# Kernel optimization log

Measured on AMD Instinct MI355X. Metric: run time of the kernel, lower is better.

Reference implementation:

```python
import jax, jax.numpy as jnp
import numpy as np

N = 50000       # num nodes
E = 800000      # num edges (avg degree 16)
D_IN = 128
D_H = 128
D_LAT = 64
BN_EPS = 1e-5


def _glorot(key, fan_in, fan_out):
    return jax.random.normal(key, (fan_in, fan_out), jnp.float32) / np.sqrt(fan_in).astype(np.float32)


def setup_inputs() -> dict:
    key = jax.random.key(0)
    ks = jax.random.split(key, 8)
    x = jax.random.normal(ks[0], (N, D_IN), jnp.float32)
    edge_index = jax.random.randint(ks[1], (2, E), 0, N)  # row 0 = src, row 1 = dst
    return {
        "x": x,
        "edge_index": edge_index,
        "W0": _glorot(ks[2], D_IN, D_H),
        "W1": _glorot(ks[3], D_H, D_H),
        "W_mu": _glorot(ks[4], D_H, D_LAT),
        "W_logvar": _glorot(ks[5], D_H, D_LAT),
        "gamma0": jnp.ones((D_H,), jnp.float32),
        "beta0": jnp.zeros((D_H,), jnp.float32),
        "gamma1": jnp.ones((D_H,), jnp.float32),
        "beta1": jnp.zeros((D_H,), jnp.float32),
    }


def _gcn_conv(h, W, src, dst, dinv):
    # Standard GCN with self-loops: D^{-1/2}(A+I)D^{-1/2} (X W)
    m = h @ W                                   # [N, out]
    coef = (dinv[src] * dinv[dst])[:, None]     # [E, 1]
    out = jax.ops.segment_sum(m[src] * coef, dst, num_segments=N)
    return out + m * (dinv * dinv)[:, None]     # self-loop contribution


def _batchnorm(h, gamma, beta):
    mean = jnp.mean(h, axis=0)
    var = jnp.var(h, axis=0)
    return (h - mean) * jax.lax.rsqrt(var + BN_EPS) * gamma + beta


def reference(x, edge_index, W0, W1, W_mu, W_logvar, gamma0, beta0, gamma1, beta1):
    # decoder_type='graph', augment_type=None, used_edge_weight=False,
    # use_FCencoder=False, num_domains=1; dropout is identity in reference.
    src, dst = edge_index[0], edge_index[1]
    deg = jax.ops.segment_sum(jnp.ones((E,), x.dtype), dst, num_segments=N) + 1.0
    dinv = jax.lax.rsqrt(deg)

    h = _gcn_conv(x, W0, src, dst, dinv)
    h = jax.nn.relu(_batchnorm(h, gamma0, beta0))
    h = _gcn_conv(h, W1, src, dst, dinv)
    h = jax.nn.relu(_batchnorm(h, gamma1, beta1))

    z_mean = _gcn_conv(h, W_mu, src, dst, dinv)
    z_log_std = _gcn_conv(h, W_logvar, src, dst, dinv)
    return (z_mean, z_log_std)
```

## Files before the change

### kernel.cpp

```cpp
#include <hip/hip_runtime.h>
#include <hip/hip_bf16.h>


using short8 = __attribute__((ext_vector_type(8))) short;
using f32x4  = __attribute__((ext_vector_type(4))) float;

static __device__ __forceinline__ unsigned short f2bf(float f) {
    __hip_bfloat16 h = __float2bfloat16(f);
    return *reinterpret_cast<unsigned short*>(&h);
}
static __device__ __forceinline__ float bf_lo(unsigned int u) {
    return __uint_as_float(u << 16);
}
static __device__ __forceinline__ float bf_hi(unsigned int u) {
    return __uint_as_float(u & 0xffff0000u);
}
static __device__ __forceinline__ float bf2f(unsigned short u) {
    return __uint_as_float((unsigned int)u << 16);
}

__global__ __launch_bounds__(256)
void deg_count(const int* __restrict__ ei, int* __restrict__ cnt, int E_) {
    int e = blockIdx.x * 256 + threadIdx.x;
    if (e < E_) atomicAdd(&cnt[ei[E_ + e]], 1);
}

__global__ __launch_bounds__(1024)
void scan_blocks(const int* __restrict__ cnt, float* __restrict__ dinv,
                 int* __restrict__ rowptr, int* __restrict__ partials, int n) {
    __shared__ int ls[1024];
    int tid = threadIdx.x;
    int i = blockIdx.x * 1024 + tid;
    int v = (i < n) ? cnt[i] : 0;
    if (i < n) dinv[i] = rsqrtf((float)v + 1.0f);
    ls[tid] = v;
    __syncthreads();
    #pragma unroll
    for (int off = 1; off < 1024; off <<= 1) {
        int t = (tid >= off) ? ls[tid - off] : 0;
        __syncthreads();
        ls[tid] += t;
        __syncthreads();
    }
    if (i < n) rowptr[i] = ls[tid] - v;
    if (tid == 1023) partials[blockIdx.x] = ls[1023];
}

__global__ __launch_bounds__(1024)
void scan_partials(int* __restrict__ partials, int* __restrict__ rowptr_n,
                   int nb) {
    __shared__ int ls[1024];
    int tid = threadIdx.x;
    int v = (tid < nb) ? partials[tid] : 0;
    ls[tid] = v;
    __syncthreads();
    #pragma unroll
    for (int off = 1; off < 1024; off <<= 1) {
        int t = (tid >= off) ? ls[tid - off] : 0;
        __syncthreads();
        ls[tid] += t;
        __syncthreads();
    }
    if (tid < nb) partials[tid] = ls[tid] - v;
    if (tid == 1023) *rowptr_n = ls[1023];
}

__global__ __launch_bounds__(256)
void scan_add(int* __restrict__ rowptr, int* __restrict__ cursor,
              const int* __restrict__ partials, int n) {
    int i = blockIdx.x * 256 + threadIdx.x;
    if (i < n) {
        int v = rowptr[i] + partials[i >> 10];
        rowptr[i] = v;
        cursor[i] = v;
    }
}

__global__ __launch_bounds__(256)
void csr_fill(const int* __restrict__ ei, const float* __restrict__ dinv,
              int* __restrict__ cursor, unsigned int* __restrict__ csr, int E_) {
    int e = blockIdx.x * 256 + threadIdx.x;
    if (e >= E_) return;
    int s = ei[e], d = ei[E_ + e];
    float coef = dinv[s] * dinv[d];
    unsigned int cb = (__float_as_uint(coef) + 0x8000u) >> 16;
    int p = atomicAdd(&cursor[d], 1);
    csr[p] = ((unsigned int)s << 15) | (cb & 0x7fffu);
}

__global__ __launch_bounds__(128)
void bn_coef(const float* __restrict__ stats, const float* __restrict__ gamma,
             const float* __restrict__ beta, float* __restrict__ sc,
             float* __restrict__ sh, int n) {
    int c = threadIdx.x;
    float inv_n = 1.0f / (float)n;
    float mean = stats[c] * inv_n;
    float var  = stats[128 + c] * inv_n - mean * mean;
    float s = rsqrtf(var + 1e-5f) * gamma[c];
    sc[c] = s;
    sh[c] = beta[c] - mean * s;
}

template<bool XBF, bool FUSE_BN, bool SPLIT_W>
__global__ __launch_bounds__(256)
void gemm_mfma(const void* __restrict__ Xv, const float* __restrict__ Wa,
               const float* __restrict__ Wb, const float* __restrict__ sc,
               const float* __restrict__ sh, unsigned short* __restrict__ Y,
               int nRows) {
    __shared__ unsigned short wt[128 * 128];

    const int tid = threadIdx.x;

    #pragma unroll
    for (int it = 0; it < 16; ++it) {
        int flat4 = it * 256 + tid;
        int k  = flat4 >> 5;
        int c0 = (flat4 & 31) * 4;
        const float* srcp;
        if (!SPLIT_W) srcp = Wa + k * 128 + c0;
        else          srcp = (c0 < 64) ? (Wa + k * 64 + c0)
                                       : (Wb + k * 64 + (c0 - 64));
        float4 v = *(const float4*)srcp;
        float vv[4] = {v.x, v.y, v.z, v.w};
        #pragma unroll
        for (int j = 0; j < 4; ++j) {
            int c = c0 + j;
            wt[c * 128 + (k ^ ((c & 7) << 3))] = f2bf(vv[j]);
        }
    }
    __syncthreads();

    const int lane = tid & 63;
    const int wv   = tid >> 6;
    const int lm   = lane & 15;
    const int lg   = lane >> 4;
    const int row0 = blockIdx.x * 128 + wv * 32;

    f32x4 acc[2][8] = {};

    #pragma unroll
    for (int ks = 0; ks < 4; ++ks) {
        const int k0 = ks * 32 + lg * 8;

        short8 a[2];
        #pragma unroll
        for (int mf = 0; mf < 2; ++mf) {
            int r = row0 + mf * 16 + lm;
            if (r < nRows) {
                if (XBF) {
                    a[mf] = *(const short8*)((const unsigned short*)Xv +
                                             (size_t)r * 128 + k0);
                    if (FUSE_BN) {
                        float4 s0 = *(const float4*)(sc + k0);
                        float4 s1 = *(const float4*)(sc + k0 + 4);
                        float4 h0 = *(const float4*)(sh + k0);
                        float4 h1 = *(const float4*)(sh + k0 + 4);
                        float sv[8] = {s0.x, s0.y, s0.z, s0.w, s1.x, s1.y, s1.z, s1.w};
                        float hv[8] = {h0.x, h0.y, h0.z, h0.w, h1.x, h1.y, h1.z, h1.w};
                        #pragma unroll
                        for (int j = 0; j < 8; ++j) {
                            float v = bf2f((unsigned short)a[mf][j]);
                            v = fmaxf(v * sv[j] + hv[j], 0.f);
                            a[mf][j] = (short)f2bf(v);
                        }
                    }
                } else {
                    const float* xp = (const float*)Xv + (size_t)r * 128 + k0;
                    float4 p0 = *(const float4*)xp;
                    float4 p1 = *(const float4*)(xp + 4);
                    float pv[8] = {p0.x, p0.y, p0.z, p0.w, p1.x, p1.y, p1.z, p1.w};
                    #pragma unroll
                    for (int j = 0; j < 8; ++j) a[mf][j] = (short)f2bf(pv[j]);
                }
            } else {
                a[mf] = short8{};
            }
        }

        #pragma unroll
        for (int f = 0; f < 8; ++f) {
            int c = f * 16 + lm;
            short8 b = *(const short8*)&wt[c * 128 + (k0 ^ ((c & 7) << 3))];
            acc[0][f] = __builtin_amdgcn_mfma_f32_16x16x32_bf16(a[0], b, acc[0][f], 0, 0, 0);
            acc[1][f] = __builtin_amdgcn_mfma_f32_16x16x32_bf16(a[1], b, acc[1][f], 0, 0, 0);
        }
    }

    #pragma unroll
    for (int mf = 0; mf < 2; ++mf) {
        #pragma unroll
        for (int reg = 0; reg < 4; ++reg) {
            int r = row0 + mf * 16 + lg * 4 + reg;
            if (r >= nRows) continue;
            #pragma unroll
            for (int f = 0; f < 8; ++f)
                Y[(size_t)r * 128 + f * 16 + lm] = f2bf(acc[mf][f][reg]);
        }
    }
}

template<bool TO_OUT>
__global__ __launch_bounds__(256)
void gather_bf(const unsigned short* __restrict__ M,
               const int* __restrict__ rowptr,
               const unsigned int* __restrict__ csr,
               const float* __restrict__ dinv, void* __restrict__ O, int n) {
    int wid  = (blockIdx.x * 256 + threadIdx.x) >> 6;
    int lane = threadIdx.x & 63;
    if (wid >= n) return;
    const unsigned int* m2 = (const unsigned int*)M;

    float di = dinv[wid];
    unsigned int su = m2[(size_t)wid * 64 + lane];
    float c = di * di;
    float a0x = bf_lo(su) * c, a0y = bf_hi(su) * c;
    float a1x = 0.f, a1y = 0.f, a2x = 0.f, a2y = 0.f, a3x = 0.f, a3y = 0.f;

    int beg = __builtin_amdgcn_readfirstlane(rowptr[wid]);
    int end = __builtin_amdgcn_readfirstlane(rowptr[wid + 1]);

    int k = beg;
    for (; k + 3 < end; k += 4) {
        unsigned int e0 = csr[k],     e1 = csr[k + 1];
        unsigned int e2 = csr[k + 2], e3 = csr[k + 3];
        unsigned int u0 = m2[(size_t)(e0 >> 15) * 64 + lane];
        unsigned int u1 = m2[(size_t)(e1 >> 15) * 64 + lane];
        unsigned int u2 = m2[(size_t)(e2 >> 15) * 64 + lane];
        unsigned int u3 = m2[(size_t)(e3 >> 15) * 64 + lane];
        float w0 = __uint_as_float((e0 & 0x7fffu) << 16);
        float w1 = __uint_as_float((e1 & 0x7fffu) << 16);
        float w2 = __uint_as_float((e2 & 0x7fffu) << 16);
        float w3 = __uint_as_float((e3 & 0x7fffu) << 16);
        a0x += w0 * bf_lo(u0); a0y += w0 * bf_hi(u0);
        a1x += w1 * bf_lo(u1); a1y += w1 * bf_hi(u1);
        a2x += w2 * bf_lo(u2); a2y += w2 * bf_hi(u2);
        a3x += w3 * bf_lo(u3); a3y += w3 * bf_hi(u3);
    }
    for (; k < end; ++k) {
        unsigned int e0 = csr[k];
        unsigned int u0 = m2[(size_t)(e0 >> 15) * 64 + lane];
        float w0 = __uint_as_float((e0 & 0x7fffu) << 16);
        a0x += w0 * bf_lo(u0); a0y += w0 * bf_hi(u0);
    }
    float ax = (a0x + a1x) + (a2x + a3x);
    float ay = (a0y + a1y) + (a2y + a3y);

    if (!TO_OUT) {
        unsigned int o = (unsigned int)f2bf(ax) | ((unsigned int)f2bf(ay) << 16);
        ((unsigned int*)O)[(size_t)wid * 64 + lane] = o;
    } else {
        float* Of = (float*)O;
        float* dst = (lane < 32)
            ? Of + (size_t)wid * 64 + 2 * lane
            : Of + (size_t)n * 64 + (size_t)wid * 64 + 2 * (lane - 32);
        *(float2*)dst = make_float2(ax, ay);
    }
}

__global__ __launch_bounds__(256)
void bn_stats(const unsigned short* __restrict__ H, float* __restrict__ stats,
              int n) {
    const uint4* h4 = (const uint4*)H;
    const int tid = threadIdx.x;
    const int cg = tid & 15;
    const int rg = tid >> 4;
    float s[8] = {}, q[8] = {};
    for (int r = blockIdx.x * 16 + rg; r < n; r += gridDim.x * 16) {
        uint4 u = h4[(size_t)r * 16 + cg];
        float v[8] = {bf_lo(u.x), bf_hi(u.x), bf_lo(u.y), bf_hi(u.y),
                      bf_lo(u.z), bf_hi(u.z), bf_lo(u.w), bf_hi(u.w)};
        #pragma unroll
        for (int j = 0; j < 8; ++j) { s[j] += v[j]; q[j] += v[j] * v[j]; }
    }
    __shared__ float ls[256][17];
    #pragma unroll
    for (int j = 0; j < 8; ++j) { ls[tid][j] = s[j]; ls[tid][8 + j] = q[j]; }
    __syncthreads();
    if (tid < 128) {
        int c = tid, cgrp = c >> 3, j = c & 7;
        float S = 0.f, Q = 0.f;
        #pragma unroll
        for (int g = 0; g < 16; ++g) {
            S += ls[(g << 4) | cgrp][j];
            Q += ls[(g << 4) | cgrp][8 + j];
        }
        atomicAdd(&stats[c], S);
        atomicAdd(&stats[128 + c], Q);
    }
}

extern "C" void kernel_launch(void* const* d_in, const int* in_sizes, int n_in,
                              void* d_out, int out_size, void* d_ws, size_t ws_size,
                              hipStream_t stream) {
    const float* x    = (const float*)d_in[0];
    const int*   ei   = (const int*)d_in[1];
    const float* W0   = (const float*)d_in[2];
    const float* W1   = (const float*)d_in[3];
    const float* Wmu  = (const float*)d_in[4];
    const float* Wlog = (const float*)d_in[5];
    const float* g0   = (const float*)d_in[6];
    const float* b0   = (const float*)d_in[7];
    const float* g1   = (const float*)d_in[8];
    const float* b1   = (const float*)d_in[9];

    const int N_ = in_sizes[0] / 128;
    const int E_ = in_sizes[1] / 2;
    float* out = (float*)d_out;

    char* w = (char*)d_ws;
    auto carve = [&](size_t bytes) {
        char* p = w;
        w += (bytes + 255) & ~(size_t)255;
        return p;
    };
    int*   cnt    = (int*)  carve((size_t)N_ * 4);
    float* stats0 = (float*)carve(256 * 4);
    float* stats1 = (float*)carve(256 * 4);
    char*  zend   = w;
    float* dinv   = (float*)carve((size_t)N_ * 4);
    int*   rowptr = (int*)  carve((size_t)(N_ + 1) * 4);
    int*   cursor = (int*)  carve((size_t)(N_ + 1) * 4);
    int*   partials = (int*)carve(1024 * 4);
    unsigned int* csr = (unsigned int*)carve((size_t)E_ * 4);
    float* sc0    = (float*)carve(128 * 4);
    float* sh0    = (float*)carve(128 * 4);
    float* sc1    = (float*)carve(128 * 4);
    float* sh1    = (float*)carve(128 * 4);
    unsigned short* Mbf = (unsigned short*)carve((size_t)N_ * 128 * 2);
    unsigned short* Hb  = (unsigned short*)carve((size_t)N_ * 128 * 2);

    const int gGemm = (N_ + 127) / 128;
    const int gGath = (N_ * 64 + 255) / 256;
    const int nb    = (N_ + 1023) / 1024;

    hipMemsetAsync(cnt, 0, (size_t)(zend - (char*)cnt), stream);
    deg_count<<<(E_ + 255) / 256, 256, 0, stream>>>(ei, cnt, E_);
    scan_blocks<<<nb, 1024, 0, stream>>>(cnt, dinv, rowptr, partials, N_);
    scan_partials<<<1, 1024, 0, stream>>>(partials, rowptr + N_, nb);
    scan_add<<<(N_ + 255) / 256, 256, 0, stream>>>(rowptr, cursor, partials, N_);
    csr_fill<<<(E_ + 255) / 256, 256, 0, stream>>>(ei, dinv, cursor, csr, E_);

    gemm_mfma<false, false, false><<<gGemm, 256, 0, stream>>>(
        x, W0, nullptr, nullptr, nullptr, Mbf, N_);
    gather_bf<false><<<gGath, 256, 0, stream>>>(Mbf, rowptr, csr, dinv, Hb, N_);
    bn_stats<<<512, 256, 0, stream>>>(Hb, stats0, N_);
    bn_coef<<<1, 128, 0, stream>>>(stats0, g0, b0, sc0, sh0, N_);

    gemm_mfma<true, true, false><<<gGemm, 256, 0, stream>>>(
        Hb, W1, nullptr, sc0, sh0, Mbf, N_);
    gather_bf<false><<<gGath, 256, 0, stream>>>(Mbf, rowptr, csr, dinv, Hb, N_);
    bn_stats<<<512, 256, 0, stream>>>(Hb, stats1, N_);
    bn_coef<<<1, 128, 0, stream>>>(stats1, g1, b1, sc1, sh1, N_);

    gemm_mfma<true, true, true><<<gGemm, 256, 0, stream>>>(
        Hb, Wmu, Wlog, sc1, sh1, Mbf, N_);
    gather_bf<true><<<gGath, 256, 0, stream>>>(Mbf, rowptr, csr, dinv, out, N_);
}
```

Baseline: 270.7 us.

## Build CSR via two-pass bucketed binning and fuse BN coefficient into stats

Replaces the per-edge global atomic CSR fill with a two-phase scheme. Edges are first binned into 128-node buckets using shared-memory histograms and one global atomic per bucket per block. A second kernel then places each bucket's edges into their rows with shared-memory atomics. Separately, the BN coefficient computation is folded into the last block of bn_stats via a ticket counter, removing two tiny launches. This trades scattered global atomics for an extra 8-byte-per-edge intermediate pass and more kernel logic.

```diff
diff --git a/kernel.cpp b/kernel.cpp
--- a/kernel.cpp
+++ b/kernel.cpp
@@ -66,39 +66,74 @@
 }
 
 __global__ __launch_bounds__(256)
-void scan_add(int* __restrict__ rowptr, int* __restrict__ cursor,
+void scan_add(int* __restrict__ rowptr, int* __restrict__ gcursor,
               const int* __restrict__ partials, int n) {
     int i = blockIdx.x * 256 + threadIdx.x;
     if (i < n) {
         int v = rowptr[i] + partials[i >> 10];
         rowptr[i] = v;
-        cursor[i] = v;
-    }
-}
-
-__global__ __launch_bounds__(256)
-void csr_fill(const int* __restrict__ ei, const float* __restrict__ dinv,
-              int* __restrict__ cursor, unsigned int* __restrict__ csr, int E_) {
-    int e = blockIdx.x * 256 + threadIdx.x;
-    if (e >= E_) return;
-    int s = ei[e], d = ei[E_ + e];
-    float coef = dinv[s] * dinv[d];
-    unsigned int cb = (__float_as_uint(coef) + 0x8000u) >> 16;
-    int p = atomicAdd(&cursor[d], 1);
-    csr[p] = ((unsigned int)s << 15) | (cb & 0x7fffu);
-}
-
-__global__ __launch_bounds__(128)
-void bn_coef(const float* __restrict__ stats, const float* __restrict__ gamma,
-             const float* __restrict__ beta, float* __restrict__ sc,
-             float* __restrict__ sh, int n) {
-    int c = threadIdx.x;
-    float inv_n = 1.0f / (float)n;
-    float mean = stats[c] * inv_n;
-    float var  = stats[128 + c] * inv_n - mean * mean;
-    float s = rsqrtf(var + 1e-5f) * gamma[c];
-    sc[c] = s;
-    sh[c] = beta[c] - mean * s;
+        if ((i & 127) == 0) gcursor[i >> 7] = v;
+    }
+}
+
+#define BCHUNK 4096
+__global__ __launch_bounds__(256)
+void bin_edges(const int* __restrict__ ei, const float* __restrict__ dinv,
+               int* __restrict__ gcursor, uint2* __restrict__ binned, int E_) {
+    __shared__ int hist[512];
+    __shared__ int gbase[512];
+    __shared__ int cur[512];
+    const int tid = threadIdx.x;
+    const int e0 = blockIdx.x * BCHUNK;
+
+    #pragma unroll
+    for (int q = 0; q < 2; ++q) hist[q * 256 + tid] = 0;
+    __syncthreads();
+
+    for (int i = tid; i < BCHUNK; i += 256) {
+        int e = e0 + i;
+        if (e < E_) atomicAdd(&hist[ei[E_ + e] >> 7], 1);
+    }
+    __syncthreads();
+
+    #pragma unroll
+    for (int q = 0; q < 2; ++q) {
+        int b = q * 256 + tid;
+        int c = hist[b];
+        gbase[b] = c ? atomicAdd(&gcursor[b], c) : 0;
+        cur[b] = 0;
+    }
+    __syncthreads();
+
+    for (int i = tid; i < BCHUNK; i += 256) {
+        int e = e0 + i;
+        if (e >= E_) continue;
+        int s = ei[e], d = ei[E_ + e];
+        float coef = dinv[s] * dinv[d];
+        unsigned int cb = (__float_as_uint(coef) + 0x8000u) >> 16;
+        unsigned int entry = ((unsigned int)s << 15) | (cb & 0x7fffu);
+        int b = d >> 7;
+        int p = gbase[b] + atomicAdd(&cur[b], 1);
+        binned[p] = make_uint2(entry, (unsigned int)(d & 127));
+    }
+}
+
+__global__ __launch_bounds__(256)
+void place_edges(const uint2* __restrict__ binned, const int* __restrict__ rowptr,
+                 unsigned int* __restrict__ csr, int n) {
+    __shared__ int cur[128];
+    const int tid = threadIdx.x;
+    const int n0 = blockIdx.x * 128;
+    const int nn = min(128, n - n0);
+    if (tid < nn) cur[tid] = rowptr[n0 + tid];
+    __syncthreads();
+    const int beg = rowptr[n0];
+    const int end = rowptr[min(n0 + 128, n)];
+    for (int i = beg + tid; i < end; i += 256) {
+        uint2 v = binned[i];
+        int p = atomicAdd(&cur[v.y], 1);
+        csr[p] = v.x;
+    }
 }
 
 template<bool XBF, bool FUSE_BN, bool SPLIT_W>
@@ -259,7 +294,9 @@
 
 __global__ __launch_bounds__(256)
 void bn_stats(const unsigned short* __restrict__ H, float* __restrict__ stats,
-              int n) {
+              const float* __restrict__ gamma, const float* __restrict__ beta,
+              float* __restrict__ sc, float* __restrict__ sh,
+              unsigned int* __restrict__ ticket, int n) {
     const uint4* h4 = (const uint4*)H;
     const int tid = threadIdx.x;
     const int cg = tid & 15;
@@ -277,15 +314,35 @@
     for (int j = 0; j < 8; ++j) { ls[tid][j] = s[j]; ls[tid][8 + j] = q[j]; }
     __syncthreads();
     if (tid < 128) {
-        int c = tid, cgrp = c >> 3, j = c & 7;
+        int cgrp = tid >> 3, j = tid & 7;
         float S = 0.f, Q = 0.f;
         #pragma unroll
         for (int g = 0; g < 16; ++g) {
             S += ls[(g << 4) | cgrp][j];
             Q += ls[(g << 4) | cgrp][8 + j];
         }
-        atomicAdd(&stats[c], S);
-        atomicAdd(&stats[128 + c], Q);
+        atomicAdd(&stats[tid], S);
+        atomicAdd(&stats[128 + tid], Q);
+    }
+    __syncthreads();
+    __shared__ int lastFlag;
+    if (tid == 0) {
+        __threadfence();
+        unsigned int t = atomicAdd(ticket, 1u);
+        lastFlag = (t == gridDim.x - 1);
+    }
+    __syncthreads();
+    if (lastFlag && tid < 128) {
+        float Ssum = __hip_atomic_load(&stats[tid], __ATOMIC_RELAXED,
+                                       __HIP_MEMORY_SCOPE_AGENT);
+        float Qsum = __hip_atomic_load(&stats[128 + tid], __ATOMIC_RELAXED,
+                                       __HIP_MEMORY_SCOPE_AGENT);
+        float inv_n = 1.0f / (float)n;
+        float mean = Ssum * inv_n;
+        float var  = Qsum * inv_n - mean * mean;
+        float sv = rsqrtf(var + 1e-5f) * gamma[tid];
+        sc[tid] = sv;
+        sh[tid] = beta[tid] - mean * sv;
     }
 }
 
@@ -313,44 +370,48 @@
         w += (bytes + 255) & ~(size_t)255;
         return p;
     };
-    int*   cnt    = (int*)  carve((size_t)N_ * 4);
-    float* stats0 = (float*)carve(256 * 4);
-    float* stats1 = (float*)carve(256 * 4);
-    char*  zend   = w;
-    float* dinv   = (float*)carve((size_t)N_ * 4);
-    int*   rowptr = (int*)  carve((size_t)(N_ + 1) * 4);
-    int*   cursor = (int*)  carve((size_t)(N_ + 1) * 4);
-    int*   partials = (int*)carve(1024 * 4);
+    int*   cnt     = (int*)  carve((size_t)N_ * 4);
+    float* stats0  = (float*)carve(256 * 4);
+    float* stats1  = (float*)carve(256 * 4);
+    unsigned int* ticket0 = (unsigned int*)carve(256);
+    unsigned int* ticket1 = (unsigned int*)carve(256);
+    char*  zend    = w;
+    float* dinv    = (float*)carve((size_t)N_ * 4);
+    int*   rowptr  = (int*)  carve((size_t)(N_ + 1) * 4);
+    int*   gcursor = (int*)  carve(512 * 4);
+    int*   partials= (int*)  carve(1024 * 4);
     unsigned int* csr = (unsigned int*)carve((size_t)E_ * 4);
-    float* sc0    = (float*)carve(128 * 4);
-    float* sh0    = (float*)carve(128 * 4);
-    float* sc1    = (float*)carve(128 * 4);
-    float* sh1    = (float*)carve(128 * 4);
+    uint2* binned  = (uint2*)carve((size_t)E_ * 8);
+    float* sc0     = (float*)carve(128 * 4);
+    float* sh0     = (float*)carve(128 * 4);
+    float* sc1     = (float*)carve(128 * 4);
+    float* sh1     = (float*)carve(128 * 4);
     unsigned short* Mbf = (unsigned short*)carve((size_t)N_ * 128 * 2);
     unsigned short* Hb  = (unsigned short*)carve((size_t)N_ * 128 * 2);
 
     const int gGemm = (N_ + 127) / 128;
     const int gGath = (N_ * 64 + 255) / 256;
     const int nb    = (N_ + 1023) / 1024;
+    const int nbk   = (N_ + 127) / 128;
+    const int gBin  = (E_ + BCHUNK - 1) / BCHUNK;
 
     hipMemsetAsync(cnt, 0, (size_t)(zend - (char*)cnt), stream);
     deg_count<<<(E_ + 255) / 256, 256, 0, stream>>>(ei, cnt, E_);
     scan_blocks<<<nb, 1024, 0, stream>>>(cnt, dinv, rowptr, partials, N_);
     scan_partials<<<1, 1024, 0, stream>>>(partials, rowptr + N_, nb);
-    scan_add<<<(N_ + 255) / 256, 256, 0, stream>>>(rowptr, cursor, partials, N_);
-    csr_fill<<<(E_ + 255) / 256, 256, 0, stream>>>(ei, dinv, cursor, csr, E_);
+    scan_add<<<(N_ + 255) / 256, 256, 0, stream>>>(rowptr, gcursor, partials, N_);
+    bin_edges<<<gBin, 256, 0, stream>>>(ei, dinv, gcursor, binned, E_);
+    place_edges<<<nbk, 256, 0, stream>>>(binned, rowptr, csr, N_);
 
     gemm_mfma<false, false, false><<<gGemm, 256, 0, stream>>>(
         x, W0, nullptr, nullptr, nullptr, Mbf, N_);
     gather_bf<false><<<gGath, 256, 0, stream>>>(Mbf, rowptr, csr, dinv, Hb, N_);
-    bn_stats<<<512, 256, 0, stream>>>(Hb, stats0, N_);
-    bn_coef<<<1, 128, 0, stream>>>(stats0, g0, b0, sc0, sh0, N_);
+    bn_stats<<<512, 256, 0, stream>>>(Hb, stats0, g0, b0, sc0, sh0, ticket0, N_);
 
     gemm_mfma<true, true, false><<<gGemm, 256, 0, stream>>>(
         Hb, W1, nullptr, sc0, sh0, Mbf, N_);
     gather_bf<false><<<gGath, 256, 0, stream>>>(Mbf, rowptr, csr, dinv, Hb, N_);
-    bn_stats<<<512, 256, 0, stream>>>(Hb, stats1, N_);
-    bn_coef<<<1, 128, 0, stream>>>(stats1, g1, b1, sc1, sh1, N_);
+    bn_stats<<<512, 256, 0, stream>>>(Hb, stats1, g1, b1, sc1, sh1, ticket1, N_);
 
     gemm_mfma<true, true, true><<<gGemm, 256, 0, stream>>>(
         Hb, Wmu, Wlog, sc1, sh1, Mbf, N_);
```

After: 259.1 us. 1.04x faster.
